# Kernel optimization log

Hardware: AMD Instinct MI355X
Metric: run time of the kernel (lower is better)

Reference implementation:

```python
import jax, jax.numpy as jnp
import numpy as np
import math

B, S, D, H = 2, 2048, 1024, 16
DH = D // H  # dim_per_head = 64


def setup_inputs() -> dict:
    key = jax.random.key(0)
    ks = jax.random.split(key, 12)
    s = 1.0 / math.sqrt(D)
    return {
        "key": jax.random.normal(ks[0], (B, S, D), jnp.float32),
        "value": jax.random.normal(ks[1], (B, S, D), jnp.float32),
        "query": jax.random.normal(ks[2], (B, S, D), jnp.float32),
        "mask": jax.random.randint(ks[3], (B, S, S), 0, 2).astype(bool),
        "Wq": jax.random.normal(ks[4], (D, D), jnp.float32) * s,
        "bq": jnp.zeros((D,), jnp.float32),
        "Wk": jax.random.normal(ks[5], (D, D), jnp.float32) * s,
        "bk": jnp.zeros((D,), jnp.float32),
        "Wv": jax.random.normal(ks[6], (D, D), jnp.float32) * s,
        "bv": jnp.zeros((D,), jnp.float32),
        "Wo": jax.random.normal(ks[7], (D, D), jnp.float32) * s,
        "bo": jnp.zeros((D,), jnp.float32),
    }


def _shape(x):
    # [B, S, D] -> [B, H, S, DH]
    return x.reshape(B, -1, H, DH).transpose(0, 2, 1, 3)


def reference(key, value, query, mask, Wq, bq, Wk, bk, Wv, bv, Wo, bo):
    q = _shape(query @ Wq.T + bq)  # [B,H,Sq,DH]
    k = _shape(key @ Wk.T + bk)    # [B,H,Sk,DH]
    v = _shape(value @ Wv.T + bv)  # [B,H,Sk,DH]
    q = q / jnp.sqrt(jnp.asarray(DH, q.dtype))
    scores = jnp.einsum("bhqd,bhkd->bhqk", q, k)
    scores = jnp.where(mask[:, None, :, :], jnp.asarray(-1e18, scores.dtype), scores)
    attn = jax.nn.softmax(scores, axis=-1)
    # dropout is identity in eval/deterministic reference
    ctx = jnp.einsum("bhqk,bhkd->bhqd", attn, v)
    ctx = ctx.transpose(0, 2, 1, 3).reshape(B, -1, D)  # unshape
    return ctx @ Wo.T + bo
```

## Files before the change

### kernel.cpp

```cpp
#include <hip/hip_runtime.h>
#include <math.h>


constexpr int Bc  = 2;
constexpr int Sc  = 2048;
constexpr int Dc  = 1024;
constexpr int Hc  = 16;
constexpr int DHc = 64;
constexpr int BSc = Bc * Sc;

constexpr float LOG2E = 1.4426950408889634f;

typedef __bf16 bf16x8 __attribute__((ext_vector_type(8)));
typedef __bf16 bf16x4 __attribute__((ext_vector_type(4)));
typedef __bf16 bf16x2 __attribute__((ext_vector_type(2)));
typedef float  f32x4  __attribute__((ext_vector_type(4)));
typedef float  f32x16 __attribute__((ext_vector_type(16)));
typedef unsigned uint32x2 __attribute__((ext_vector_type(2)));
typedef unsigned uint32x4 __attribute__((ext_vector_type(4)));

#define GLDS16(gp, lp) __builtin_amdgcn_global_load_lds( \
    (const __attribute__((address_space(1))) void*)(gp), \
    (__attribute__((address_space(3))) void*)(lp), 16, 0, 0)

__global__ __launch_bounds__(256)
void wsplit(const float* __restrict__ W0, const float* __restrict__ W1,
            const float* __restrict__ W2, const float* __restrict__ W3,
            __bf16* __restrict__ out)
{
    const float* src[4] = {W0, W1, W2, W3};
    const int z = blockIdx.y;
    const size_t idx = ((size_t)blockIdx.x * 256 + threadIdx.x) * 4;
    const float4 v = *(const float4*)&src[z][idx];
    bf16x4 o;
    o[0] = (__bf16)v.x; o[1] = (__bf16)v.y; o[2] = (__bf16)v.z; o[3] = (__bf16)v.w;
    *(bf16x4*)&out[(size_t)z * Dc * Dc + idx] = o;
}

__device__ __forceinline__ void sweep128p(const float* __restrict__ A,
                                          const __bf16* __restrict__ Wh,
                                          char* AsB, char* WsB,
                                          int gm0, int gn0, f32x4 acc[4][4])
{
    const int tid  = threadIdx.x;
    const int w    = tid >> 6;
    const int lane = tid & 63;
    const int cc   = lane & 15;
    const int g    = lane >> 4;
    const int wm   = (w & 1) * 64;
    const int wn   = (w >> 1) * 64;

    int wrow[4], wchk[4];
#pragma unroll
    for (int r = 0; r < 4; ++r) {
        const int L = r * 256 + tid;
        wrow[r] = L >> 3;
        wchk[r] = (L & 7) ^ (wrow[r] & 7);
    }

    float4 av[8];
#pragma unroll
    for (int r = 0; r < 4; ++r)
        GLDS16(Wh + (size_t)(gn0 + wrow[r]) * Dc + wchk[r] * 8,
               WsB + (r * 256 + tid) * 16);
#pragma unroll
    for (int i = 0; i < 8; ++i) {
        const int Lq = i * 256 + tid;
        av[i] = *(const float4*)&A[(size_t)(gm0 + (Lq >> 4)) * Dc + (Lq & 15) * 4];
    }
#pragma unroll
    for (int i = 0; i < 8; ++i) {
        const int Lq = i * 256 + tid;
        const int ar = Lq >> 4, aq = Lq & 15;
        const int off = ar * 128 + ((((aq >> 1) ^ (ar & 7)) << 4) | ((aq & 1) << 3));
        bf16x4 hv;
        hv[0] = (__bf16)av[i].x; hv[1] = (__bf16)av[i].y;
        hv[2] = (__bf16)av[i].z; hv[3] = (__bf16)av[i].w;
        *(bf16x4*)(AsB + off) = hv;
    }

    for (int it = 0; it < Dc / 64; ++it) {
        const char* As = AsB + (it & 1) * 16384;
        const char* Ws = WsB + (it & 1) * 16384;
        __syncthreads();

        const bool more = (it + 1 < Dc / 64);
        if (more) {
            const int kn = (it + 1) * 64;
            char* Wn = WsB + ((it + 1) & 1) * 16384;
#pragma unroll
            for (int r = 0; r < 4; ++r)
                GLDS16(Wh + (size_t)(gn0 + wrow[r]) * Dc + kn + wchk[r] * 8,
                       Wn + (r * 256 + tid) * 16);
#pragma unroll
            for (int i = 0; i < 8; ++i) {
                const int Lq = i * 256 + tid;
                av[i] = *(const float4*)
                    &A[(size_t)(gm0 + (Lq >> 4)) * Dc + kn + (Lq & 15) * 4];
            }
        }

#pragma unroll
        for (int kk = 0; kk < 2; ++kk) {
            const int cb4 = (kk * 4 + g) << 4;
            bf16x8 af[4], bfr[4];
#pragma unroll
            for (int mt = 0; mt < 4; ++mt) {
                const int row = wm + mt * 16 + cc;
                af[mt] = *(const bf16x8*)(As + row * 128 + (cb4 ^ ((row & 7) << 4)));
            }
#pragma unroll
            for (int nt = 0; nt < 4; ++nt) {
                const int row = wn + nt * 16 + cc;
                bfr[nt] = *(const bf16x8*)(Ws + row * 128 + (cb4 ^ ((row & 7) << 4)));
            }
#pragma unroll
            for (int mt = 0; mt < 4; ++mt)
#pragma unroll
                for (int nt = 0; nt < 4; ++nt)
                    acc[mt][nt] = __builtin_amdgcn_mfma_f32_16x16x32_bf16(
                        af[mt], bfr[nt], acc[mt][nt], 0, 0, 0);
        }

        if (more) {
            char* An = AsB + ((it + 1) & 1) * 16384;
#pragma unroll
            for (int i = 0; i < 8; ++i) {
                const int Lq = i * 256 + tid;
                const int ar = Lq >> 4, aq = Lq & 15;
                const int off = ar * 128 +
                                ((((aq >> 1) ^ (ar & 7)) << 4) | ((aq & 1) << 3));
                bf16x4 hv;
                hv[0] = (__bf16)av[i].x; hv[1] = (__bf16)av[i].y;
                hv[2] = (__bf16)av[i].z; hv[3] = (__bf16)av[i].w;
                *(bf16x4*)(An + off) = hv;
            }
        }
    }
}

__device__ __forceinline__ void sweep64p(const __bf16* __restrict__ Ahi,
                                         const __bf16* __restrict__ Alo,
                                         const __bf16* __restrict__ Wh,
                                         char* WsB, char* AhB, char* AlB,
                                         int gm0, int gn0, f32x4 acc[2][4])
{
    const int tid  = threadIdx.x;
    const int w    = tid >> 6;
    const int lane = tid & 63;
    const int cc   = lane & 15;
    const int g    = lane >> 4;
    const int wm   = (w & 1) * 32;
    const int wn   = (w >> 1) * 64;

    int wrow[4], wchk[4];
#pragma unroll
    for (int r = 0; r < 4; ++r) {
        const int L = r * 256 + tid;
        wrow[r] = L >> 3;
        wchk[r] = (L & 7) ^ (wrow[r] & 7);
    }
    int arow[2], achk[2];
#pragma unroll
    for (int r = 0; r < 2; ++r) {
        const int L = r * 256 + tid;
        arow[r] = L >> 3;
        achk[r] = (L & 7) ^ (arow[r] & 7);
    }

#pragma unroll
    for (int r = 0; r < 4; ++r)
        GLDS16(Wh + (size_t)(gn0 + wrow[r]) * Dc + wchk[r] * 8,
               WsB + (r * 256 + tid) * 16);
#pragma unroll
    for (int r = 0; r < 2; ++r) {
        GLDS16(Ahi + (size_t)(gm0 + arow[r]) * Dc + achk[r] * 8,
               AhB + (r * 256 + tid) * 16);
        GLDS16(Alo + (size_t)(gm0 + arow[r]) * Dc + achk[r] * 8,
               AlB + (r * 256 + tid) * 16);
    }

    for (int it = 0; it < Dc / 64; ++it) {
        const char* Ws = WsB + (it & 1) * 16384;
        const char* Ah = AhB + (it & 1) * 8192;
        const char* Al = AlB + (it & 1) * 8192;
        __syncthreads();

        if (it + 1 < Dc / 64) {
            const int kn = (it + 1) * 64;
            char* Wn = WsB + ((it + 1) & 1) * 16384;
            char* Hn = AhB + ((it + 1) & 1) * 8192;
            char* Ln = AlB + ((it + 1) & 1) * 8192;
#pragma unroll
            for (int r = 0; r < 4; ++r)
                GLDS16(Wh + (size_t)(gn0 + wrow[r]) * Dc + kn + wchk[r] * 8,
                       Wn + (r * 256 + tid) * 16);
#pragma unroll
            for (int r = 0; r < 2; ++r) {
                GLDS16(Ahi + (size_t)(gm0 + arow[r]) * Dc + kn + achk[r] * 8,
                       Hn + (r * 256 + tid) * 16);
                GLDS16(Alo + (size_t)(gm0 + arow[r]) * Dc + kn + achk[r] * 8,
                       Ln + (r * 256 + tid) * 16);
            }
        }

#pragma unroll
        for (int kk = 0; kk < 2; ++kk) {
            const int cb4 = (kk * 4 + g) << 4;
            bf16x8 ahi[2], alo[2], bfr[4];
#pragma unroll
            for (int mt = 0; mt < 2; ++mt) {
                const int row = wm + mt * 16 + cc;
                const int off = row * 128 + (cb4 ^ ((row & 7) << 4));
                ahi[mt] = *(const bf16x8*)(Ah + off);
                alo[mt] = *(const bf16x8*)(Al + off);
            }
#pragma unroll
            for (int nt = 0; nt < 4; ++nt) {
                const int row = wn + nt * 16 + cc;
                bfr[nt] = *(const bf16x8*)(Ws + row * 128 + (cb4 ^ ((row & 7) << 4)));
            }
#pragma unroll
            for (int mt = 0; mt < 2; ++mt)
#pragma unroll
                for (int nt = 0; nt < 4; ++nt) {
                    acc[mt][nt] = __builtin_amdgcn_mfma_f32_16x16x32_bf16(
                        ahi[mt], bfr[nt], acc[mt][nt], 0, 0, 0);
                    acc[mt][nt] = __builtin_amdgcn_mfma_f32_16x16x32_bf16(
                        alo[mt], bfr[nt], acc[mt][nt], 0, 0, 0);
                }
        }
    }
}

__global__ __launch_bounds__(256)
void qkv_mfma(const float* __restrict__ query, const float* __restrict__ key,
              const float* __restrict__ value, const __bf16* __restrict__ Whi,
              const float* __restrict__ bq, const float* __restrict__ bk,
              const float* __restrict__ bv,
              __bf16* __restrict__ Qo, __bf16* __restrict__ Ko, __bf16* __restrict__ Vt)
{
    __shared__ __align__(16) char smem[65536];

    const int z = blockIdx.z;
    const float* A    = (z == 0) ? query : (z == 1) ? key : value;
    const float* bias = (z == 0) ? bq    : (z == 1) ? bk  : bv;
    const float scale = (z == 0) ? 0.125f * LOG2E : 1.0f;
    const __bf16* Wh  = Whi + (size_t)z * Dc * Dc;

    const int gm0 = blockIdx.x * 128;
    const int gn0 = blockIdx.y * 128;

    f32x4 acc[4][4];
#pragma unroll
    for (int mt = 0; mt < 4; ++mt)
#pragma unroll
        for (int nt = 0; nt < 4; ++nt) acc[mt][nt] = {0.f, 0.f, 0.f, 0.f};

    sweep128p(A, Wh, smem, smem + 32768, gm0, gn0, acc);

    const int tid = threadIdx.x;
    const int w = tid >> 6, lane = tid & 63;
    const int cc = lane & 15, g = lane >> 4;
    const int wm = (w & 1) * 64, wn = (w >> 1) * 64;

    float bias4[4];
#pragma unroll
    for (int nt = 0; nt < 4; ++nt) bias4[nt] = bias[gn0 + wn + nt * 16 + cc];

    if (z == 2) {
#pragma unroll
        for (int mt = 0; mt < 4; ++mt)
#pragma unroll
            for (int nt = 0; nt < 4; ++nt) {
                const int col = gn0 + wn + nt * 16 + cc;
                const int h = col >> 6, dh = col & 63;
                const int row0 = gm0 + wm + mt * 16 + g * 4;
                const int b = row0 >> 11, s0 = row0 & 2047;
                bf16x4 vv;
#pragma unroll
                for (int reg = 0; reg < 4; ++reg)
                    vv[reg] = (__bf16)(acc[mt][nt][reg] + bias4[nt]);
                *(bf16x4*)&Vt[(((size_t)(b * Hc + h)) * DHc + dh) * Sc + s0] = vv;
            }
    } else {
        __bf16* O = (z == 0) ? Qo : Ko;
#pragma unroll
        for (int mt = 0; mt < 4; ++mt)
#pragma unroll
            for (int nt = 0; nt < 4; ++nt) {
                const int col = gn0 + wn + nt * 16 + cc;
                const int h = col >> 6, dh = col & 63;
#pragma unroll
                for (int reg = 0; reg < 4; ++reg) {
                    const int row = gm0 + wm + mt * 16 + g * 4 + reg;
                    const int b = row >> 11, s = row & 2047;
                    O[(((size_t)(b * Hc + h)) * Sc + s) * DHc + dh] =
                        (__bf16)((acc[mt][nt][reg] + bias4[nt]) * scale);
                }
            }
    }
}

__global__ __launch_bounds__(256)
void out_mfma(const __bf16* __restrict__ ctxHi, const __bf16* __restrict__ ctxLo,
              const __bf16* __restrict__ Wohi,
              const float* __restrict__ bo, float* __restrict__ out)
{
    __shared__ __align__(16) char smem[65536];

    const int gm0 = blockIdx.x * 64;
    const int gn0 = blockIdx.y * 128;

    f32x4 acc[2][4];
#pragma unroll
    for (int mt = 0; mt < 2; ++mt)
#pragma unroll
        for (int nt = 0; nt < 4; ++nt) acc[mt][nt] = {0.f, 0.f, 0.f, 0.f};

    sweep64p(ctxHi, ctxLo, Wohi, smem, smem + 32768, smem + 49152, gm0, gn0, acc);

    const int tid = threadIdx.x;
    const int w = tid >> 6, lane = tid & 63;
    const int cc = lane & 15, g = lane >> 4;
    const int wm = (w & 1) * 32, wn = (w >> 1) * 64;

    float bias4[4];
#pragma unroll
    for (int nt = 0; nt < 4; ++nt) bias4[nt] = bo[gn0 + wn + nt * 16 + cc];

#pragma unroll
    for (int mt = 0; mt < 2; ++mt)
#pragma unroll
        for (int nt = 0; nt < 4; ++nt) {
            const int col = gn0 + wn + nt * 16 + cc;
#pragma unroll
            for (int reg = 0; reg < 4; ++reg) {
                const int row = gm0 + wm + mt * 16 + g * 4 + reg;
                out[(size_t)row * Dc + col] = acc[mt][nt][reg] + bias4[nt];
            }
        }
}

__global__ __launch_bounds__(256)
void mask_pack(const int* __restrict__ mask, unsigned long long* __restrict__ out)
{
    const int lane = threadIdx.x & 63;
    const size_t waveBase = ((size_t)blockIdx.x * 4 + (threadIdx.x >> 6)) * 256;
    unsigned long long b0 = __ballot(mask[waveBase + lane]        != 0);
    unsigned long long b1 = __ballot(mask[waveBase + 64 + lane]   != 0);
    unsigned long long b2 = __ballot(mask[waveBase + 128 + lane]  != 0);
    unsigned long long b3 = __ballot(mask[waveBase + 192 + lane]  != 0);
    if (lane == 0) {
        unsigned long long* dst = out + (waveBase >> 6);
        dst[0] = b0; dst[1] = b1; dst[2] = b2; dst[3] = b3;
    }
}

__global__ __launch_bounds__(256, 2)
void attn_mfma(const __bf16* __restrict__ Q, const __bf16* __restrict__ K,
               const __bf16* __restrict__ Vt,
               const unsigned long long* __restrict__ mp,
               __bf16* __restrict__ ctxHi, __bf16* __restrict__ ctxLo)
{
    __shared__ __align__(16) char smem[32768];

    const int tid  = threadIdx.x;
    const int w    = tid >> 6;
    const int lane = tid & 63;
    const int c    = lane & 31;
    const int u    = lane >> 5;
    const int bh   = blockIdx.y;
    const int b    = bh >> 4;
    const int h    = bh & 15;
    const int qw   = blockIdx.x * 128 + w * 32;

    const __bf16* Qb  = Q  + (size_t)bh * Sc * DHc;
    const __bf16* Kb  = K  + (size_t)bh * Sc * DHc;
    const __bf16* Vtb = Vt + (size_t)bh * DHc * Sc;

    bf16x8 qa[4];
#pragma unroll
    for (int ch = 0; ch < 4; ++ch)
        qa[ch] = *(const bf16x8*)&Qb[(size_t)(qw + c) * DHc + ch * 16 + u * 8];

    f32x16 o[2];
#pragma unroll
    for (int dt = 0; dt < 2; ++dt)
#pragma unroll
        for (int i = 0; i < 16; ++i) o[dt][i] = 0.f;
    float lp[4] = {0.f, 0.f, 0.f, 0.f};

    const int ci[2] = {tid, 256 + tid};
    int rowi[2], ski[2];
#pragma unroll
    for (int i = 0; i < 2; ++i) {
        rowi[i] = ci[i] >> 3;
        ski[i]  = (ci[i] & 7) ^ (rowi[i] & 7);
    }

#pragma unroll
    for (int i = 0; i < 2; ++i) {
        GLDS16(Kb + (size_t)rowi[i] * DHc + ski[i] * 8,
               smem + ci[i] * 16);
        GLDS16(Vtb + (size_t)rowi[i] * Sc + ski[i] * 8,
               smem + 8192 + ci[i] * 16);
    }

    for (int it = 0; it < 32; ++it) {
        const char* Ks = smem + (it & 1) * 16384;
        const char* Vs = Ks + 8192;

        __syncthreads();

        if (it + 1 < 32) {
            char* Kn = smem + ((it + 1) & 1) * 16384;
            const int kn = (it + 1) * 64;
#pragma unroll
            for (int i = 0; i < 2; ++i) {
                GLDS16(Kb + (size_t)(kn + rowi[i]) * DHc + ski[i] * 8,
                       Kn + ci[i] * 16);
                GLDS16(Vtb + (size_t)rowi[i] * Sc + kn + ski[i] * 8,
                       Kn + 8192 + ci[i] * 16);
            }
        }

        const unsigned long long mw =
            mp[((size_t)(b * Sc + qw + c) << 5) + it];

        f32x16 sc[2];
        __builtin_amdgcn_s_setprio(1);
#pragma unroll
        for (int nt = 0; nt < 2; ++nt) {
            f32x16 z;
#pragma unroll
            for (int i = 0; i < 16; ++i) z[i] = -24.f;
#pragma unroll
            for (int ch = 0; ch < 4; ++ch) {
                const int row = nt * 32 + c;
                const bf16x8 kb = *(const bf16x8*)
                    (Ks + row * 128 + ((ch * 32 + u * 16) ^ ((row & 7) << 4)));
                z = __builtin_amdgcn_mfma_f32_32x32x16_bf16(kb, qa[ch], z, 0, 0, 0);
            }
            sc[nt] = z;
        }
        __builtin_amdgcn_s_setprio(0);

        unsigned pk[2][4][2];
#pragma unroll
        for (int nt = 0; nt < 2; ++nt)
#pragma unroll
            for (int rr = 0; rr < 4; ++rr) {
                const unsigned nib =
                    (unsigned)(mw >> (nt * 32 + rr * 8 + u * 4)) & 0xFu;
                float pv[4];
#pragma unroll
                for (int r = 0; r < 4; ++r) {
                    float p = __builtin_amdgcn_exp2f(sc[nt][rr * 4 + r]);
                    p = (nib & (1u << r)) ? 0.f : p;
                    lp[rr] += p;
                    pv[r] = p;
                }
                bf16x2 t0; t0[0] = (__bf16)pv[0]; t0[1] = (__bf16)pv[1];
                bf16x2 t1; t1[0] = (__bf16)pv[2]; t1[1] = (__bf16)pv[3];
                pk[nt][rr][0] = __builtin_bit_cast(unsigned, t0);
                pk[nt][rr][1] = __builtin_bit_cast(unsigned, t1);
            }

        bf16x8 pa[4];
#pragma unroll
        for (int kc = 0; kc < 4; ++kc) {
            const int nt = kc >> 1;
            const int r0 = (kc & 1) * 2;
            uint32x2 s0 = __builtin_amdgcn_permlane32_swap(
                pk[nt][r0][0], pk[nt][r0 + 1][0], false, false);
            uint32x2 s1 = __builtin_amdgcn_permlane32_swap(
                pk[nt][r0][1], pk[nt][r0 + 1][1], false, false);
            uint32x4 wds;
            wds[0] = s0[0]; wds[1] = s1[0]; wds[2] = s0[1]; wds[3] = s1[1];
            pa[kc] = __builtin_bit_cast(bf16x8, wds);
        }

        __builtin_amdgcn_s_setprio(1);
#pragma unroll
        for (int dt = 0; dt < 2; ++dt)
#pragma unroll
            for (int kc = 0; kc < 4; ++kc) {
                const int row = dt * 32 + c;
                const bf16x8 vb = *(const bf16x8*)
                    (Vs + row * 128 + ((kc * 32 + u * 16) ^ ((row & 7) << 4)));
                o[dt] = __builtin_amdgcn_mfma_f32_32x32x16_bf16(pa[kc], vb, o[dt], 0, 0, 0);
            }
        __builtin_amdgcn_s_setprio(0);
    }

    float lsum = (lp[0] + lp[1]) + (lp[2] + lp[3]);
    lsum += __shfl_xor(lsum, 32);
    const float linv = 1.0f / lsum;

    float inv[16];
#pragma unroll
    for (int i = 0; i < 16; ++i)
        inv[i] = __shfl(linv, (i & 3) + 8 * (i >> 2) + 4 * u);

#pragma unroll
    for (int dt = 0; dt < 2; ++dt)
#pragma unroll
        for (int i = 0; i < 16; ++i) {
            const int q = qw + (i & 3) + 8 * (i >> 2) + 4 * u;
            const size_t idx = ((size_t)b * Sc + q) * Dc + h * 64 + dt * 32 + c;
            const float v = o[dt][i] * inv[i];
            const __bf16 hi = (__bf16)v;
            ctxHi[idx] = hi;
            ctxLo[idx] = (__bf16)(v - (float)hi);
        }
}

extern "C" void kernel_launch(void* const* d_in, const int* in_sizes, int n_in,
                              void* d_out, int out_size, void* d_ws, size_t ws_size,
                              hipStream_t stream)
{
    const float* key   = (const float*)d_in[0];
    const float* value = (const float*)d_in[1];
    const float* query = (const float*)d_in[2];
    const int*   mask  = (const int*)  d_in[3];
    const float* Wq    = (const float*)d_in[4];
    const float* bq    = (const float*)d_in[5];
    const float* Wk    = (const float*)d_in[6];
    const float* bk    = (const float*)d_in[7];
    const float* Wv    = (const float*)d_in[8];
    const float* bv    = (const float*)d_in[9];
    const float* Wo    = (const float*)d_in[10];
    const float* bo    = (const float*)d_in[11];
    float* out = (float*)d_out;

    char* wsb = (char*)d_ws;
    __bf16* Qbf  = (__bf16*)(wsb);
    __bf16* Kbf  = (__bf16*)(wsb + ((size_t)8  << 20));
    __bf16* Vt   = (__bf16*)(wsb + ((size_t)16 << 20));
    unsigned long long* mpk = (unsigned long long*)(wsb + ((size_t)32 << 20));
    __bf16* Whi  = (__bf16*)(wsb + ((size_t)33 << 20));
    __bf16* ctxHi = (__bf16*)(wsb + ((size_t)41 << 20));
    __bf16* ctxLo = (__bf16*)(wsb + ((size_t)49 << 20));

    dim3 gws(Dc * Dc / (256 * 4), 4);
    wsplit<<<gws, 256, 0, stream>>>(Wq, Wk, Wv, Wo, Whi);

    dim3 gqkv(BSc / 128, Dc / 128, 3);
    qkv_mfma<<<gqkv, 256, 0, stream>>>(query, key, value, Whi, bq, bk, bv,
                                       Qbf, Kbf, Vt);

    const int mask_n = Bc * Sc * Sc;
    mask_pack<<<mask_n / 1024, 256, 0, stream>>>(mask, mpk);

    dim3 gattn(Sc / 128, Bc * Hc);
    attn_mfma<<<gattn, 256, 0, stream>>>(Qbf, Kbf, Vt, mpk, ctxHi, ctxLo);

    dim3 gout(BSc / 64, Dc / 128);
    out_mfma<<<gout, 256, 0, stream>>>(ctxHi, ctxLo, Whi + (size_t)3 * Dc * Dc,
                                       bo, out);
}
```

Measured before the change: 272.8 us.

## Pre-cast QKV activations to bf16 and stream them via direct-to-LDS loads

After: 251.1 us. 1.09x faster.

```diff
diff --git a/kernel.cpp b/kernel.cpp
--- a/kernel.cpp
+++ b/kernel.cpp
@@ -37,10 +37,25 @@
     *(bf16x4*)&out[(size_t)z * Dc * Dc + idx] = o;
 }
 
-__device__ __forceinline__ void sweep128p(const float* __restrict__ A,
-                                          const __bf16* __restrict__ Wh,
-                                          char* AsB, char* WsB,
-                                          int gm0, int gn0, f32x4 acc[4][4])
+__global__ __launch_bounds__(256)
+void acast(const float* __restrict__ A0, const float* __restrict__ A1,
+           const float* __restrict__ A2, __bf16* __restrict__ out)
+{
+    const float* src[3] = {A0, A1, A2};
+    const int z = blockIdx.y;
+    const size_t idx = ((size_t)blockIdx.x * 256 + threadIdx.x) * 8;
+    const float4 a = *(const float4*)&src[z][idx];
+    const float4 b = *(const float4*)&src[z][idx + 4];
+    bf16x8 o;
+    o[0] = (__bf16)a.x; o[1] = (__bf16)a.y; o[2] = (__bf16)a.z; o[3] = (__bf16)a.w;
+    o[4] = (__bf16)b.x; o[5] = (__bf16)b.y; o[6] = (__bf16)b.z; o[7] = (__bf16)b.w;
+    *(bf16x8*)&out[(size_t)z * BSc * Dc + idx] = o;
+}
+
+__device__ __forceinline__ void sweep128bb(const __bf16* __restrict__ A,
+                                           const __bf16* __restrict__ Wh,
+                                           char* AsB, char* WsB,
+                                           int gm0, int gn0, f32x4 acc[4][4])
 {
     const int tid  = threadIdx.x;
     const int w    = tid >> 6;
@@ -58,25 +73,12 @@
         wchk[r] = (L & 7) ^ (wrow[r] & 7);
     }
 
-    float4 av[8];
-#pragma unroll
-    for (int r = 0; r < 4; ++r)
+#pragma unroll
+    for (int r = 0; r < 4; ++r) {
         GLDS16(Wh + (size_t)(gn0 + wrow[r]) * Dc + wchk[r] * 8,
                WsB + (r * 256 + tid) * 16);
-#pragma unroll
-    for (int i = 0; i < 8; ++i) {
-        const int Lq = i * 256 + tid;
-        av[i] = *(const float4*)&A[(size_t)(gm0 + (Lq >> 4)) * Dc + (Lq & 15) * 4];
-    }
-#pragma unroll
-    for (int i = 0; i < 8; ++i) {
-        const int Lq = i * 256 + tid;
-        const int ar = Lq >> 4, aq = Lq & 15;
-        const int off = ar * 128 + ((((aq >> 1) ^ (ar & 7)) << 4) | ((aq & 1) << 3));
-        bf16x4 hv;
-        hv[0] = (__bf16)av[i].x; hv[1] = (__bf16)av[i].y;
-        hv[2] = (__bf16)av[i].z; hv[3] = (__bf16)av[i].w;
-        *(bf16x4*)(AsB + off) = hv;
+        GLDS16(A + (size_t)(gm0 + wrow[r]) * Dc + wchk[r] * 8,
+               AsB + (r * 256 + tid) * 16);
     }
 
     for (int it = 0; it < Dc / 64; ++it) {
@@ -84,22 +86,20 @@
         const char* Ws = WsB + (it & 1) * 16384;
         __syncthreads();
 
-        const bool more = (it + 1 < Dc / 64);
-        if (more) {
+        if (it + 1 < Dc / 64) {
             const int kn = (it + 1) * 64;
             char* Wn = WsB + ((it + 1) & 1) * 16384;
-#pragma unroll
-            for (int r = 0; r < 4; ++r)
+            char* An = AsB + ((it + 1) & 1) * 16384;
+#pragma unroll
+            for (int r = 0; r < 4; ++r) {
                 GLDS16(Wh + (size_t)(gn0 + wrow[r]) * Dc + kn + wchk[r] * 8,
                        Wn + (r * 256 + tid) * 16);
-#pragma unroll
-            for (int i = 0; i < 8; ++i) {
-                const int Lq = i * 256 + tid;
-                av[i] = *(const float4*)
-                    &A[(size_t)(gm0 + (Lq >> 4)) * Dc + kn + (Lq & 15) * 4];
-            }
-        }
-
+                GLDS16(A + (size_t)(gm0 + wrow[r]) * Dc + kn + wchk[r] * 8,
+                       An + (r * 256 + tid) * 16);
+            }
+        }
+
+        __builtin_amdgcn_s_setprio(1);
 #pragma unroll
         for (int kk = 0; kk < 2; ++kk) {
             const int cb4 = (kk * 4 + g) << 4;
@@ -121,21 +121,7 @@
                     acc[mt][nt] = __builtin_amdgcn_mfma_f32_16x16x32_bf16(
                         af[mt], bfr[nt], acc[mt][nt], 0, 0, 0);
         }
-
-        if (more) {
-            char* An = AsB + ((it + 1) & 1) * 16384;
-#pragma unroll
-            for (int i = 0; i < 8; ++i) {
-                const int Lq = i * 256 + tid;
-                const int ar = Lq >> 4, aq = Lq & 15;
-                const int off = ar * 128 +
-                                ((((aq >> 1) ^ (ar & 7)) << 4) | ((aq & 1) << 3));
-                bf16x4 hv;
-                hv[0] = (__bf16)av[i].x; hv[1] = (__bf16)av[i].y;
-                hv[2] = (__bf16)av[i].z; hv[3] = (__bf16)av[i].w;
-                *(bf16x4*)(An + off) = hv;
-            }
-        }
+        __builtin_amdgcn_s_setprio(0);
     }
 }
 
@@ -234,8 +220,7 @@
 }
 
 __global__ __launch_bounds__(256)
-void qkv_mfma(const float* __restrict__ query, const float* __restrict__ key,
-              const float* __restrict__ value, const __bf16* __restrict__ Whi,
+void qkv_mfma(const __bf16* __restrict__ Abf, const __bf16* __restrict__ Whi,
               const float* __restrict__ bq, const float* __restrict__ bk,
               const float* __restrict__ bv,
               __bf16* __restrict__ Qo, __bf16* __restrict__ Ko, __bf16* __restrict__ Vt)
@@ -243,9 +228,9 @@
     __shared__ __align__(16) char smem[65536];
 
     const int z = blockIdx.z;
-    const float* A    = (z == 0) ? query : (z == 1) ? key : value;
-    const float* bias = (z == 0) ? bq    : (z == 1) ? bk  : bv;
+    const float* bias = (z == 0) ? bq : (z == 1) ? bk : bv;
     const float scale = (z == 0) ? 0.125f * LOG2E : 1.0f;
+    const __bf16* A   = Abf + (size_t)z * BSc * Dc;
     const __bf16* Wh  = Whi + (size_t)z * Dc * Dc;
 
     const int gm0 = blockIdx.x * 128;
@@ -257,7 +242,7 @@
 #pragma unroll
         for (int nt = 0; nt < 4; ++nt) acc[mt][nt] = {0.f, 0.f, 0.f, 0.f};
 
-    sweep128p(A, Wh, smem, smem + 32768, gm0, gn0, acc);
+    sweep128bb(A, Wh, smem, smem + 32768, gm0, gn0, acc);
 
     const int tid = threadIdx.x;
     const int w = tid >> 6, lane = tid & 63;
@@ -542,13 +527,16 @@
     __bf16* Whi  = (__bf16*)(wsb + ((size_t)33 << 20));
     __bf16* ctxHi = (__bf16*)(wsb + ((size_t)41 << 20));
     __bf16* ctxLo = (__bf16*)(wsb + ((size_t)49 << 20));
+    __bf16* Abf  = (__bf16*)(wsb + ((size_t)57 << 20));
 
     dim3 gws(Dc * Dc / (256 * 4), 4);
     wsplit<<<gws, 256, 0, stream>>>(Wq, Wk, Wv, Wo, Whi);
 
+    dim3 gac(BSc * Dc / (256 * 8), 3);
+    acast<<<gac, 256, 0, stream>>>(query, key, value, Abf);
+
     dim3 gqkv(BSc / 128, Dc / 128, 3);
-    qkv_mfma<<<gqkv, 256, 0, stream>>>(query, key, value, Whi, bq, bk, bv,
-                                       Qbf, Kbf, Vt);
+    qkv_mfma<<<gqkv, 256, 0, stream>>>(Abf, Whi, bq, bk, bv, Qbf, Kbf, Vt);
 
     const int mask_n = Bc * Sc * Sc;
     mask_pack<<<mask_n / 1024, 256, 0, stream>>>(mask, mpk);
```
